# Kernel optimization log

Measured on AMD Instinct MI355X. Metric: run time of the kernel, lower is better.

The kernel has to match this reference:

```python
import jax, jax.numpy as jnp
import numpy as np

VOCAB_SIZE = 256
CODEC_VOCAB = 1024  # 2 ** codec_bits
D = 1024
NHEAD = 16
FF = 4096
L = 6
ENROLLED = 225  # enrolled_codec_sec(3) * codec_rate(75)
B, TT, TA = 4, 128, 512


def sinusoidal_pe(T, d):
    pos = np.arange(T, dtype=np.float32)[:, None]
    div = np.exp(np.arange(0, d, 2, dtype=np.float32) * (-np.log(10000.0) / d))
    pe = np.zeros((T, d), dtype=np.float32)
    pe[:, 0::2] = np.sin(pos * div)
    pe[:, 1::2] = np.cos(pos * div)
    return jnp.asarray(pe)


def layernorm(x, w, b, eps=1e-5):
    mu = x.mean(-1, keepdims=True)
    var = ((x - mu) ** 2).mean(-1, keepdims=True)
    return (x - mu) * jax.lax.rsqrt(var + eps) * w + b


def mha(q_in, kv_in, in_w, in_b, out_w, out_b, mask=None):
    # q_in: [B,Tq,D], kv_in: [B,Tk,D]; mask True == blocked (torch attn_mask convention)
    d = q_in.shape[-1]
    h, hd = NHEAD, d // NHEAD
    wq, wk, wv = in_w[:d], in_w[d:2 * d], in_w[2 * d:]
    bq, bk, bv = in_b[:d], in_b[d:2 * d], in_b[2 * d:]
    Bq, Tq, _ = q_in.shape
    Tk = kv_in.shape[1]
    q = (q_in @ wq.T + bq).reshape(Bq, Tq, h, hd)
    k = (kv_in @ wk.T + bk).reshape(Bq, Tk, h, hd)
    v = (kv_in @ wv.T + bv).reshape(Bq, Tk, h, hd)
    scores = jnp.einsum('bqhd,bkhd->bhqk', q, k) / jnp.sqrt(jnp.float32(hd))
    if mask is not None:
        scores = jnp.where(mask, -jnp.inf, scores)
    attn = jax.nn.softmax(scores, axis=-1)
    o = jnp.einsum('bhqk,bkhd->bqhd', attn, v).reshape(Bq, Tq, d)
    return o @ out_w.T + out_b


def pack(te, ae, ee, tl, al):
    # Ragged concat [text[:tl]; audio[:al]; enrolled] padded to static max_len.
    Tt, Ta, Te = te.shape[0], ae.shape[0], ee.shape[0]
    pos = jnp.arange(Tt + Ta + Te)
    t = te[jnp.clip(pos, 0, Tt - 1)]
    a = ae[jnp.clip(pos - tl, 0, Ta - 1)]
    e = ee[jnp.clip(pos - tl - al, 0, Te - 1)]
    x = jnp.where((pos < tl)[:, None], t,
        jnp.where((pos < tl + al)[:, None], a,
        jnp.where((pos < tl + al + Te)[:, None], e, jnp.zeros_like(t))))
    return x


def setup_inputs():
    key = jax.random.key(0)
    ks = iter(jax.random.split(key, 64))

    def n(shape, s=0.02):
        return jax.random.normal(next(ks), shape, dtype=jnp.float32) * s

    text = jax.random.randint(next(ks), (B, TT), 0, VOCAB_SIZE)
    audio = jax.random.randint(next(ks), (B, TA), 0, CODEC_VOCAB)
    enrolled_audio = jax.random.randint(next(ks), (B, ENROLLED), 0, CODEC_VOCAB)
    # force sample 0 to full length so max_len is static (= TT+TA+ENROLLED)
    text_len_batch = jax.random.randint(next(ks), (B,), TT // 2, TT + 1).at[0].set(TT)
    audio_len_batch = jax.random.randint(next(ks), (B,), TA // 2, TA + 1).at[0].set(TA)
    return dict(
        text=text, audio=audio, enrolled_audio=enrolled_audio,
        text_len_batch=text_len_batch, audio_len_batch=audio_len_batch,
        text_emb=n((VOCAB_SIZE, D)), audio_emb=n((CODEC_VOCAB, D)),
        sa_in_w=n((L, 3 * D, D)), sa_in_b=jnp.zeros((L, 3 * D), jnp.float32),
        sa_out_w=n((L, D, D)), sa_out_b=jnp.zeros((L, D), jnp.float32),
        ca_in_w=n((L, 3 * D, D)), ca_in_b=jnp.zeros((L, 3 * D), jnp.float32),
        ca_out_w=n((L, D, D)), ca_out_b=jnp.zeros((L, D), jnp.float32),
        ff1_w=n((L, FF, D)), ff1_b=jnp.zeros((L, FF), jnp.float32),
        ff2_w=n((L, D, FF)), ff2_b=jnp.zeros((L, D), jnp.float32),
        ln1_w=jnp.ones((L, D), jnp.float32), ln1_b=jnp.zeros((L, D), jnp.float32),
        ln2_w=jnp.ones((L, D), jnp.float32), ln2_b=jnp.zeros((L, D), jnp.float32),
        ln3_w=jnp.ones((L, D), jnp.float32), ln3_b=jnp.zeros((L, D), jnp.float32),
        out_w=n((CODEC_VOCAB, D)), out_b=jnp.zeros((CODEC_VOCAB,), jnp.float32))


def reference(text, audio, enrolled_audio, text_len_batch, audio_len_batch,
              text_emb, audio_emb, sa_in_w, sa_in_b, sa_out_w, sa_out_b,
              ca_in_w, ca_in_b, ca_out_w, ca_out_b, ff1_w, ff1_b, ff2_w, ff2_b,
              ln1_w, ln1_b, ln2_w, ln2_b, ln3_w, ln3_b, out_w, out_b):
    # per-segment sinusoidal PE (positions reset at the start of each segment)
    te = text_emb[text] + sinusoidal_pe(text.shape[1], D)
    ae = audio_emb[audio] + sinusoidal_pe(audio.shape[1], D)
    ee = audio_emb[enrolled_audio] + sinusoidal_pe(enrolled_audio.shape[1], D)
    embed = jax.vmap(pack)(te, ae, ee, text_len_batch, audio_len_batch)  # [B, max_len, D]
    max_len = embed.shape[1]
    prefix = text.shape[1] + audio.shape[1]  # == max(tl+al) by construction
    mask = jnp.triu(jnp.ones((max_len, max_len), bool), 1).at[:, :prefix].set(False)
    mem = embed  # TransformerDecoder memory == embed
    x = embed
    for l in range(L):  # post-norm decoder layers (torch default norm_first=False)
        x = layernorm(x + mha(x, x, sa_in_w[l], sa_in_b[l], sa_out_w[l], sa_out_b[l], mask), ln1_w[l], ln1_b[l])
        x = layernorm(x + mha(x, mem, ca_in_w[l], ca_in_b[l], ca_out_w[l], ca_out_b[l]), ln2_w[l], ln2_b[l])
        h = jax.nn.relu(x @ ff1_w[l].T + ff1_b[l]) @ ff2_w[l].T + ff2_b[l]
        x = layernorm(x + h, ln3_w[l], ln3_b[l])
    return x @ out_w.T + out_b  # [B, max_len, CODEC_VOCAB]
```

## Files before the change

kernel.cpp:

```cpp
#include <hip/hip_runtime.h>
#include <hip/hip_bf16.h>

#define B_      4
#define TT_     128
#define TA_     512
#define TE_     225
#define T_      865
#define D_      1024
#define H_      16
#define FF_     4096
#define L_      6
#define PREFIX_ 640
#define M_TOK   (B_ * T_)
#define M_PAD   3584
#define NKV     (L_ * 2 * D_)

typedef __attribute__((ext_vector_type(8))) short          s16x8;
typedef __attribute__((ext_vector_type(4))) float          f32x4;
typedef __attribute__((ext_vector_type(8))) unsigned short u16x8;

typedef __attribute__((address_space(1))) const void gv_t;
typedef __attribute__((address_space(3))) void       lv_t;

__device__ __forceinline__ float bf2f(unsigned short u) {
  union { unsigned int i; float f; } c; c.i = ((unsigned int)u) << 16; return c.f;
}
__device__ __forceinline__ unsigned short f2bf(float f) {
  union { __hip_bfloat16 h; unsigned short u; } c; c.h = __float2bfloat16(f); return c.u;
}
template <int N> __device__ __forceinline__ void vmwait() {
  asm volatile("s_waitcnt vmcnt(%0)" :: "n"(N) : "memory");
}

__global__ __launch_bounds__(256) void embed_kernel(
    const int* __restrict__ text, const int* __restrict__ audio,
    const int* __restrict__ enrolled, const int* __restrict__ tl_b,
    const int* __restrict__ al_b, const float* __restrict__ text_emb,
    const float* __restrict__ audio_emb,
    unsigned short* __restrict__ xb,
    unsigned short* __restrict__ memb, unsigned short* __restrict__ attnb) {
  int row = blockIdx.x;
  int d0 = threadIdx.x * 4;
  size_t off = (size_t)row * D_ + d0;
  if (row >= M_TOK) {
    *(unsigned long long*)&xb[off]    = 0ull;
    *(unsigned long long*)&memb[off]  = 0ull;
    *(unsigned long long*)&attnb[off] = 0ull;
    return;
  }
  int b = row / T_, pos = row - b * T_;
  int tl = tl_b[b], al = al_b[b];
  const float* emb = nullptr;
  int p = 0;
  if (pos < tl) {
    emb = text_emb + (size_t)text[b * TT_ + pos] * D_;
    p = pos;
  } else if (pos < tl + al) {
    emb = audio_emb + (size_t)audio[b * TA_ + (pos - tl)] * D_;
    p = pos - tl;
  } else if (pos < tl + al + TE_) {
    emb = audio_emb + (size_t)enrolled[b * TE_ + (pos - tl - al)] * D_;
    p = pos - tl - al;
  }
  float4 v;
  float* pv = (float*)&v;
  if (emb) {
    const float c = -9.2103403719761836f / (float)D_;
    #pragma unroll
    for (int e = 0; e < 4; ++e) {
      int d = d0 + e;
      int i = d >> 1;
      float freq = expf(c * (float)(2 * i));
      float arg = (float)p * freq;
      float pe = (d & 1) ? cosf(arg) : sinf(arg);
      pv[e] = emb[d] + pe;
    }
  } else {
    v = make_float4(0.f, 0.f, 0.f, 0.f);
  }
  unsigned long long pk = (unsigned long long)f2bf(pv[0])
      | ((unsigned long long)f2bf(pv[1]) << 16)
      | ((unsigned long long)f2bf(pv[2]) << 32)
      | ((unsigned long long)f2bf(pv[3]) << 48);
  *(unsigned long long*)&xb[off]   = pk;
  *(unsigned long long*)&memb[off] = pk;
}

__global__ __launch_bounds__(256) void cvt_kernel(
    const float* __restrict__ in, unsigned short* __restrict__ out, int n8) {
  int i = blockIdx.x * 256 + threadIdx.x;
  if (i >= n8) return;
  const float4* pp = (const float4*)in + (size_t)i * 2;
  float4 a = pp[0], bq = pp[1];
  u16x8 o;
  o[0] = f2bf(a.x);  o[1] = f2bf(a.y);  o[2] = f2bf(a.z);  o[3] = f2bf(a.w);
  o[4] = f2bf(bq.x); o[5] = f2bf(bq.y); o[6] = f2bf(bq.z); o[7] = f2bf(bq.w);
  *(u16x8*)(out + (size_t)i * 8) = o;
}

__global__ __launch_bounds__(256) void cvt_layer_kernel(
    const float* __restrict__ s0, const float* __restrict__ s1,
    const float* __restrict__ s2, const float* __restrict__ s3,
    const float* __restrict__ s4, const float* __restrict__ s5,
    unsigned short* __restrict__ dst) {
  size_t e = ((size_t)blockIdx.x * 256 + threadIdx.x) * 8;
  if (e >= 16777216u) return;
  const float* src; size_t off;
  if      (e <  3145728u) { src = s0; off = e; }
  else if (e <  4194304u) { src = s1; off = e -  3145728u; }
  else if (e <  7340032u) { src = s2; off = e -  4194304u; }
  else if (e <  8388608u) { src = s3; off = e -  7340032u; }
  else if (e < 12582912u) { src = s4; off = e -  8388608u; }
  else                    { src = s5; off = e - 12582912u; }
  const float4* pp = (const float4*)(src + off);
  float4 a = pp[0], bq = pp[1];
  u16x8 o;
  o[0] = f2bf(a.x);  o[1] = f2bf(a.y);  o[2] = f2bf(a.z);  o[3] = f2bf(a.w);
  o[4] = f2bf(bq.x); o[5] = f2bf(bq.y); o[6] = f2bf(bq.z); o[7] = f2bf(bq.w);
  *(u16x8*)(dst + e) = o;
}

__global__ __launch_bounds__(256) void cvt_ckv_w(
    const float* __restrict__ ca_in_w, unsigned short* __restrict__ wckv) {
  int rr = blockIdx.x;
  int l = rr / (2 * D_), w = rr % (2 * D_);
  const float* src = ca_in_w + (size_t)l * 3 * D_ * D_ + (size_t)(D_ + w) * D_;
  unsigned short* dst = wckv + (size_t)rr * D_;
  int c = threadIdx.x * 4;
  float4 v4 = *(const float4*)(src + c);
  unsigned long long pk = (unsigned long long)f2bf(v4.x)
      | ((unsigned long long)f2bf(v4.y) << 16)
      | ((unsigned long long)f2bf(v4.z) << 32)
      | ((unsigned long long)f2bf(v4.w) << 48);
  *(unsigned long long*)&dst[c] = pk;
}

__global__ __launch_bounds__(256) void cvt_ckv_b(
    const float* __restrict__ ca_in_b, float* __restrict__ cbias) {
  int rr = blockIdx.x * 256 + threadIdx.x;
  if (rr >= NKV) return;
  int l = rr / (2 * D_), w = rr % (2 * D_);
  cbias[rr] = ca_in_b[(size_t)l * 3 * D_ + D_ + w];
}

template <int ACT, int OBF, int NSTRIPE>
__global__ __launch_bounds__(512, 2) void gemm_8w(
    const unsigned short* __restrict__ A, int lda,
    const unsigned short* __restrict__ W, int ldw,
    const float* __restrict__ bias,
    float* __restrict__ Cf, unsigned short* __restrict__ Cb, int ldc,
    int Mw, int K) {
  __shared__ unsigned short lds[2][2][256 * 64];
  int tid = threadIdx.x, lane = tid & 63, wid = tid >> 6;

  int gx = gridDim.x;
  int nwg = gx * gridDim.y;
  int orig = blockIdx.y * gx + blockIdx.x;
  int m0, n0;
  if (NSTRIPE && (gx & 7) == 0) {
    int stripe = gx >> 3;
    int xcd = orig & 7, loc = orig >> 3;
    n0 = (xcd * stripe + loc % stripe) * 256;
    m0 = (loc / stripe) * 256;
  } else {
    int q = nwg >> 3, r = nwg & 7;
    int xcd = orig & 7, loc = orig >> 3;
    int wg = (xcd < r ? xcd * (q + 1) : r * (q + 1) + (xcd - r) * q) + loc;
    m0 = (wg / gx) * 256;
    n0 = (wg % gx) * 256;
  }

  int wr = wid >> 2, wc = wid & 3;
  int r16 = lane & 15, g4 = lane >> 4;

  int srow = lane >> 3;
  int sgrp = (lane & 7) ^ srow;
  const unsigned short* gA[4];
  const unsigned short* gB[4];
  unsigned soff[4];
  #pragma unroll
  for (int c = 0; c < 4; ++c) {
    int rb = wid * 32 + c * 8;
    gA[c] = A + (size_t)(m0 + rb + srow) * lda + sgrp * 8;
    gB[c] = W + (size_t)(n0 + rb + srow) * ldw + sgrp * 8;
    soff[c] = rb * 64;
  }

  f32x4 acc[8][4];
  #pragma unroll
  for (int i = 0; i < 8; ++i)
    #pragma unroll
    for (int j = 0; j < 4; ++j) acc[i][j] = (f32x4)0.f;

  auto STAGE = [&](int bi, int t) {
    int k0 = t * 64;
    #pragma unroll
    for (int c = 0; c < 4; ++c)
      __builtin_amdgcn_global_load_lds((gv_t*)(gA[c] + k0),
          (lv_t*)&lds[bi][0][soff[c]], 16, 0, 0);
    #pragma unroll
    for (int c = 0; c < 4; ++c)
      __builtin_amdgcn_global_load_lds((gv_t*)(gB[c] + k0),
          (lv_t*)&lds[bi][1][soff[c]], 16, 0, 0);
  };

  STAGE(0, 0);
  int nt = K / 64, cur = 0;
  for (int t = 0; t < nt; ++t) {
    vmwait<0>();
    __builtin_amdgcn_s_barrier();
    if (t + 1 < nt) STAGE(cur ^ 1, t + 1);

    const unsigned short* Ab = &lds[cur][0][0];
    const unsigned short* Bb = &lds[cur][1][0];

    s16x8 bf_[4][2];
    #pragma unroll
    for (int j = 0; j < 4; ++j)
      #pragma unroll
      for (int kk = 0; kk < 2; ++kk) {
        int row = wc * 64 + j * 16 + r16;
        bf_[j][kk] = *(const s16x8*)&Bb[row * 64 + (((kk * 4 + g4) ^ (row & 7)) * 8)];
      }

    #pragma unroll
    for (int p = 0; p < 4; ++p) {
      s16x8 af_[2][2];
      #pragma unroll
      for (int ii = 0; ii < 2; ++ii)
        #pragma unroll
        for (int kk = 0; kk < 2; ++kk) {
          int row = wr * 128 + (p * 2 + ii) * 16 + r16;
          af_[ii][kk] = *(const s16x8*)&Ab[row * 64 + (((kk * 4 + g4) ^ (row & 7)) * 8)];
        }
      __builtin_amdgcn_s_setprio(1);
      #pragma unroll
      for (int kk = 0; kk < 2; ++kk)
        #pragma unroll
        for (int ii = 0; ii < 2; ++ii)
          #pragma unroll
          for (int j = 0; j < 4; ++j)
            acc[p * 2 + ii][j] = __builtin_amdgcn_mfma_f32_16x16x32_bf16(
                af_[ii][kk], bf_[j][kk], acc[p * 2 + ii][j], 0, 0, 0);
      __builtin_amdgcn_s_setprio(0);
    }
    cur ^= 1;
  }

  float bv[4];
  #pragma unroll
  for (int j = 0; j < 4; ++j) bv[j] = bias[n0 + wc * 64 + j * 16 + r16];
  int rbase = m0 + wr * 128 + g4 * 4;
  int cbase = n0 + wc * 64 + r16;
  #pragma unroll
  for (int i = 0; i < 8; ++i)
    #pragma unroll
    for (int rr = 0; rr < 4; ++rr) {
      int m = rbase + i * 16 + rr;
      if (m < Mw) {
        #pragma unroll
        for (int j = 0; j < 4; ++j) {
          float v = acc[i][j][rr] + bv[j];
          if (ACT) v = fmaxf(v, 0.f);
          if (OBF) Cb[(size_t)m * ldc + cbase + j * 16] = f2bf(v);
          else     Cf[(size_t)m * ldc + cbase + j * 16] = v;
        }
      }
    }
}

template <int ACT, int OBF, int NSTRIPE>
__global__ __launch_bounds__(512, 2) void gemm_8w128(
    const unsigned short* __restrict__ A, int lda,
    const unsigned short* __restrict__ W, int ldw,
    const float* __restrict__ bias,
    float* __restrict__ Cf, unsigned short* __restrict__ Cb, int ldc,
    int Mw, int K) {
  __shared__ unsigned short lds[2][2][128 * 64];
  int tid = threadIdx.x, lane = tid & 63, wid = tid >> 6;

  int gx = gridDim.x;
  int nwg = gx * gridDim.y;
  int orig = blockIdx.y * gx + blockIdx.x;
  int m0, n0;
  if (NSTRIPE && (gx & 7) == 0) {
    int stripe = gx >> 3;
    int xcd = orig & 7, loc = orig >> 3;
    n0 = (xcd * stripe + loc % stripe) * 128;
    m0 = (loc / stripe) * 128;
  } else {
    int q = nwg >> 3, r = nwg & 7;
    int xcd = orig & 7, loc = orig >> 3;
    int wg = (xcd < r ? xcd * (q + 1) : r * (q + 1) + (xcd - r) * q) + loc;
    m0 = (wg / gx) * 128;
    n0 = (wg % gx) * 128;
  }

  int wr = wid >> 2, wc = wid & 3;
  int r16 = lane & 15, g4 = lane >> 4;

  int srow = lane >> 3;
  int sgrp = (lane & 7) ^ srow;
  const unsigned short* gA[2];
  const unsigned short* gB[2];
  unsigned soff[2];
  #pragma unroll
  for (int c = 0; c < 2; ++c) {
    int rb = wid * 16 + c * 8;
    gA[c] = A + (size_t)(m0 + rb + srow) * lda + sgrp * 8;
    gB[c] = W + (size_t)(n0 + rb + srow) * ldw + sgrp * 8;
    soff[c] = rb * 64;
  }

  f32x4 acc[4][2];
  #pragma unroll
  for (int i = 0; i < 4; ++i)
    #pragma unroll
    for (int j = 0; j < 2; ++j) acc[i][j] = (f32x4)0.f;

  auto STAGE = [&](int bi, int t) {
    int k0 = t * 64;
    #pragma unroll
    for (int c = 0; c < 2; ++c)
      __builtin_amdgcn_global_load_lds((gv_t*)(gA[c] + k0),
          (lv_t*)&lds[bi][0][soff[c]], 16, 0, 0);
    #pragma unroll
    for (int c = 0; c < 2; ++c)
      __builtin_amdgcn_global_load_lds((gv_t*)(gB[c] + k0),
          (lv_t*)&lds[bi][1][soff[c]], 16, 0, 0);
  };

  STAGE(0, 0);
  int nt = K / 64, cur = 0;
  for (int t = 0; t < nt; ++t) {
    vmwait<0>();
    __builtin_amdgcn_s_barrier();
    if (t + 1 < nt) STAGE(cur ^ 1, t + 1);

    const unsigned short* Ab = &lds[cur][0][0];
    const unsigned short* Bb = &lds[cur][1][0];

    s16x8 bf_[2][2];
    #pragma unroll
    for (int j = 0; j < 2; ++j)
      #pragma unroll
      for (int kk = 0; kk < 2; ++kk) {
        int row = wc * 32 + j * 16 + r16;
        bf_[j][kk] = *(const s16x8*)&Bb[row * 64 + (((kk * 4 + g4) ^ (row & 7)) * 8)];
      }
    s16x8 af_[4][2];
    #pragma unroll
    for (int ii = 0; ii < 4; ++ii)
      #pragma unroll
      for (int kk = 0; kk < 2; ++kk) {
        int row = wr * 64 + ii * 16 + r16;
        af_[ii][kk] = *(const s16x8*)&Ab[row * 64 + (((kk * 4 + g4) ^ (row & 7)) * 8)];
      }
    __builtin_amdgcn_s_setprio(1);
    #pragma unroll
    for (int kk = 0; kk < 2; ++kk)
      #pragma unroll
      for (int ii = 0; ii < 4; ++ii)
        #pragma unroll
        for (int j = 0; j < 2; ++j)
          acc[ii][j] = __builtin_amdgcn_mfma_f32_16x16x32_bf16(
              af_[ii][kk], bf_[j][kk], acc[ii][j], 0, 0, 0);
    __builtin_amdgcn_s_setprio(0);
    cur ^= 1;
  }

  float bv[2];
  #pragma unroll
  for (int j = 0; j < 2; ++j) bv[j] = bias[n0 + wc * 32 + j * 16 + r16];
  int rbase = m0 + wr * 64 + g4 * 4;
  int cbase = n0 + wc * 32 + r16;
  #pragma unroll
  for (int i = 0; i < 4; ++i)
    #pragma unroll
    for (int rr = 0; rr < 4; ++rr) {
      int m = rbase + i * 16 + rr;
      if (m < Mw) {
        #pragma unroll
        for (int j = 0; j < 2; ++j) {
          float v = acc[i][j][rr] + bv[j];
          if (ACT) v = fmaxf(v, 0.f);
          if (OBF) Cb[(size_t)m * ldc + cbase + j * 16] = f2bf(v);
          else     Cf[(size_t)m * ldc + cbase + j * 16] = v;
        }
      }
    }
}

template <int BM, int BN, int BK, int ACT, int OBF, int NSTRIPE>
__global__ __launch_bounds__(256) void gemm_p2(
    const unsigned short* __restrict__ A, int lda,
    const unsigned short* __restrict__ W, int ldw,
    const float* __restrict__ bias,
    float* __restrict__ Cf, unsigned short* __restrict__ Cb, int ldc,
    int Mw, int K) {
  constexpr int WROWS = BM / 2, WCOLS = BN / 2;
  constexpr int WM = WROWS / 16, WN = WCOLS / 16;
  constexpr int LPR = BK / 8;
  constexpr int RPI = 64 / LPR;
  constexpr int ACH = (BM / 4) / RPI;
  constexpr int BCH = (BN / 4) / RPI;
  constexpr int ABUF = BM * BK, BBUF = BN * BK;
  constexpr int KSUB = BK / 32;
  constexpr int LW = ACH + BCH;
  __shared__ unsigned short lds[3 * (ABUF + BBUF)];

  int tid = threadIdx.x, lane = tid & 63, wid = tid >> 6;
  int gx = gridDim.x;
  int nwg = gx * gridDim.y;
  int orig = blockIdx.y * gx + blockIdx.x;
  int m0, n0;
  if (NSTRIPE && (gx & 7) == 0) {
    int stripe = gx >> 3;
    int xcd = orig & 7, loc = orig >> 3;
    n0 = (xcd * stripe + loc % stripe) * BN;
    m0 = (loc / stripe) * BM;
  } else {
    int q = nwg >> 3, r = nwg & 7;
    int xcd = orig & 7, loc = orig >> 3;
    int wg = (xcd < r ? xcd * (q + 1) : r * (q + 1) + (xcd - r) * q) + loc;
    m0 = (wg / gx) * BM;
    n0 = (wg % gx) * BN;
  }

  int wr = wid >> 1, wc = wid & 1;
  int lrow = lane / LPR, lgrp = lane % LPR;
  int skey = (BK == 32) ? ((lrow >> 1) & 3) : (lrow & 7);
  int lk = (lgrp ^ skey) * 8;

  const unsigned short* gAp[ACH]; unsigned aoff[ACH];
  const unsigned short* gBp[BCH]; unsigned boff[BCH];
  #pragma unroll
  for (int c = 0; c < ACH; ++c) {
    int row0 = wid * (BM / 4) + c * RPI;
    gAp[c] = A + (size_t)(m0 + row0 + lrow) * lda + lk;
    aoff[c] = row0 * BK;
  }
  #pragma unroll
  for (int c = 0; c < BCH; ++c) {
    int row0 = wid * (BN / 4) + c * RPI;
    gBp[c] = W + (size_t)(n0 + row0 + lrow) * ldw + lk;
    boff[c] = row0 * BK;
  }

  f32x4 acc[WM][WN];
  #pragma unroll
  for (int i = 0; i < WM; ++i)
    #pragma unroll
    for (int j = 0; j < WN; ++j) acc[i][j] = (f32x4)0.f;

  int frow = lane & 15, g4 = lane >> 4;

  auto STAGE = [&](int bi, int t) {
    int k0 = t * BK;
    #pragma unroll
    for (int c = 0; c < ACH; ++c)
      __builtin_amdgcn_global_load_lds((gv_t*)(gAp[c] + k0),
          (lv_t*)&lds[bi * ABUF + aoff[c]], 16, 0, 0);
    #pragma unroll
    for (int c = 0; c < BCH; ++c)
      __builtin_amdgcn_global_load_lds((gv_t*)(gBp[c] + k0),
          (lv_t*)&lds[3 * ABUF + bi * BBUF + boff[c]], 16, 0, 0);
  };

  STAGE(0, 0);
  STAGE(1, 1);
  int nt = K / BK;
  int cur = 0;
  for (int t = 0; t < nt; ++t) {
    if (t + 1 < nt) vmwait<LW>(); else vmwait<0>();
    __builtin_amdgcn_s_barrier();
    if (t + 2 < nt) {
      int stb = cur + 2; if (stb >= 3) stb -= 3;
      STAGE(stb, t + 2);
    }
    const unsigned short* Ab = &lds[cur * ABUF];
    const unsigned short* Bb = &lds[3 * ABUF + cur * BBUF];
    #pragma unroll
    for (int kk = 0; kk < KSUB; ++kk) {
      int rk = (BK == 32) ? ((g4 ^ ((frow >> 1) & 3)) * 8)
                          : (((kk * 4 + g4) ^ (frow & 7)) * 8);
      s16x8 af[WM], bfr[WN];
      #pragma unroll
      for (int i = 0; i < WM; ++i)
        af[i] = *(const s16x8*)&Ab[(wr * WROWS + i * 16 + frow) * BK + rk];
      #pragma unroll
      for (int j = 0; j < WN; ++j)
        bfr[j] = *(const s16x8*)&Bb[(wc * WCOLS + j * 16 + frow) * BK + rk];
      __builtin_amdgcn_s_setprio(1);
      #pragma unroll
      for (int i = 0; i < WM; ++i)
        #pragma unroll
        for (int j = 0; j < WN; ++j)
          acc[i][j] = __builtin_amdgcn_mfma_f32_16x16x32_bf16(af[i], bfr[j], acc[i][j], 0, 0, 0);
      __builtin_amdgcn_s_setprio(0);
    }
    cur = (cur == 2) ? 0 : cur + 1;
  }

  float bv[WN];
  #pragma unroll
  for (int j = 0; j < WN; ++j) bv[j] = bias[n0 + wc * WCOLS + j * 16 + (lane & 15)];
  int rbase = m0 + wr * WROWS + (lane >> 4) * 4;
  int cbase = n0 + wc * WCOLS + (lane & 15);
  #pragma unroll
  for (int i = 0; i < WM; ++i)
    #pragma unroll
    for (int rr = 0; rr < 4; ++rr) {
      int m = rbase + i * 16 + rr;
      if (m < Mw) {
        #pragma unroll
        for (int j = 0; j < WN; ++j) {
          float v = acc[i][j][rr] + bv[j];
          if (ACT) v = fmaxf(v, 0.f);
          if (OBF) Cb[(size_t)m * ldc + cbase + j * 16] = f2bf(v);
          else     Cf[(size_t)m * ldc + cbase + j * 16] = v;
        }
      }
    }
}

template <bool MASKED>
__global__ __launch_bounds__(512, 2) void attn_mfma(
    const unsigned short* __restrict__ qp, int qld,
    const unsigned short* __restrict__ kp,
    const unsigned short* __restrict__ vp, int kvld,
    unsigned short* __restrict__ out) {
  __shared__ unsigned short KsL[64 * 64];
  __shared__ unsigned short VtL[64 * 72];
  __shared__ unsigned short PsL[8][16 * 64];
  int tid = threadIdx.x;
  int lane = tid & 63, wid = tid >> 6;
  int b = blockIdx.y >> 4, h = blockIdx.y & 15;
  int q0 = blockIdx.x * 128;
  int r16 = lane & 15, g4 = lane >> 4;

  int qrow = q0 + wid * 16 + r16;
  if (qrow >= T_) qrow = T_ - 1;
  const unsigned short* qbase =
      qp + (size_t)(b * T_ + qrow) * qld + h * 64 + g4 * 8;
  s16x8 qf0 = *(const s16x8*)qbase;
  s16x8 qf1 = *(const s16x8*)(qbase + 32);

  float m_[4], l_[4];
  f32x4 o_[4];
  #pragma unroll
  for (int rg = 0; rg < 4; ++rg) { m_[rg] = -INFINITY; l_[rg] = 0.f; }
  #pragma unroll
  for (int dj = 0; dj < 4; ++dj) o_[dj] = (f32x4)0.f;

  int qmax = q0 + 127;

  for (int t = 0; t < 14; ++t) {
    int k0 = t * 64;
    if (MASKED && k0 > qmax && k0 >= PREFIX_) break;
    __syncthreads();

    {
      int row = wid * 8 + (lane >> 3);
      int kr = k0 + row; if (kr >= T_) kr = T_ - 1;
      int grp = (lane & 7) ^ (row & 7);
      const unsigned short* src =
          kp + (size_t)(b * T_ + kr) * kvld + h * 64 + grp * 8;
      __builtin_amdgcn_global_load_lds((gv_t*)src,
          (lv_t*)&KsL[(wid * 8) * 64], 16, 0, 0);
    }
    {
      int vkr = k0 + lane; if (vkr >= T_) vkr = T_ - 1;
      const unsigned short* vsrc =
          vp + (size_t)(b * T_ + vkr) * kvld + h * 64 + wid * 8;
      u16x8 v0 = *(const u16x8*)vsrc;
      #pragma unroll
      for (int jj = 0; jj < 8; ++jj)
        VtL[(wid * 8 + jj) * 72 + lane] = v0[jj];
    }
    __syncthreads();

    f32x4 sj[4];
    #pragma unroll
    for (int j = 0; j < 4; ++j) sj[j] = (f32x4)0.f;
    __builtin_amdgcn_s_setprio(1);
    #pragma unroll
    for (int j = 0; j < 4; ++j) {
      int krow = j * 16 + r16;
      s16x8 kf0 = *(const s16x8*)&KsL[krow * 64 + ((g4 ^ (krow & 7)) * 8)];
      s16x8 kf1 = *(const s16x8*)&KsL[krow * 64 + (((4 + g4) ^ (krow & 7)) * 8)];
      sj[j] = __builtin_amdgcn_mfma_f32_16x16x32_bf16(qf0, kf0, sj[j], 0, 0, 0);
      sj[j] = __builtin_amdgcn_mfma_f32_16x16x32_bf16(qf1, kf1, sj[j], 0, 0, 0);
    }
    __builtin_amdgcn_s_setprio(0);

    float alpha_[4];
    #pragma unroll
    for (int rg = 0; rg < 4; ++rg) {
      int qa = q0 + wid * 16 + g4 * 4 + rg;
      float pm = -INFINITY;
      #pragma unroll
      for (int j = 0; j < 4; ++j) {
        int kg = k0 + j * 16 + r16;
        float sv = sj[j][rg] * 0.125f;
        bool bad = (kg >= T_) || (MASKED && kg > qa && kg >= PREFIX_);
        sv = bad ? -INFINITY : sv;
        sj[j][rg] = sv;
        pm = fmaxf(pm, sv);
      }
      pm = fmaxf(pm, __shfl_xor(pm, 1));
      pm = fmaxf(pm, __shfl_xor(pm, 2));
      pm = fmaxf(pm, __shfl_xor(pm, 4));
      pm = fmaxf(pm, __shfl_xor(pm, 8));
      float mn = fmaxf(m_[rg], pm);
      float al = __expf(m_[rg] - mn);
      m_[rg] = mn;
      alpha_[rg] = al;
      int prow = g4 * 4 + rg;
      float ps = 0.f;
      #pragma unroll
      for (int j = 0; j < 4; ++j) {
        float pv = __expf(sj[j][rg] - mn);
        ps += pv;
        PsL[wid][prow * 64 + (((j * 2 + (r16 >> 3)) ^ (prow & 7)) * 8) + (r16 & 7)]
            = f2bf(pv);
      }
      ps += __shfl_xor(ps, 1);
      ps += __shfl_xor(ps, 2);
      ps += __shfl_xor(ps, 4);
      ps += __shfl_xor(ps, 8);
      l_[rg] = l_[rg] * al + ps;
    }
    #pragma unroll
    for (int dj = 0; dj < 4; ++dj)
      #pragma unroll
      for (int rg = 0; rg < 4; ++rg) o_[dj][rg] *= alpha_[rg];

    __builtin_amdgcn_s_setprio(1);
    #pragma unroll
    for (int kk = 0; kk < 2; ++kk) {
      s16x8 pf = *(const s16x8*)
          &PsL[wid][r16 * 64 + (((kk * 4 + g4) ^ (r16 & 7)) * 8)];
      #pragma unroll
      for (int dj = 0; dj < 4; ++dj) {
        s16x8 vf = *(const s16x8*)
            &VtL[(dj * 16 + r16) * 72 + kk * 32 + g4 * 8];
        o_[dj] = __builtin_amdgcn_mfma_f32_16x16x32_bf16(pf, vf, o_[dj], 0, 0, 0);
      }
    }
    __builtin_amdgcn_s_setprio(0);
  }

  #pragma unroll
  for (int rg = 0; rg < 4; ++rg) {
    int qa = q0 + wid * 16 + g4 * 4 + rg;
    if (qa < T_) {
      float inv = 1.f / l_[rg];
      unsigned short* ob = out + (size_t)(b * T_ + qa) * D_ + h * 64;
      #pragma unroll
      for (int dj = 0; dj < 4; ++dj)
        ob[dj * 16 + r16] = f2bf(o_[dj][rg] * inv);
    }
  }
}

__global__ __launch_bounds__(256) void ln_res_kernel(
    unsigned short* __restrict__ xb, const unsigned short* __restrict__ r,
    const float* __restrict__ w, const float* __restrict__ b) {
  __shared__ float red[4];
  int row = blockIdx.x, tid = threadIdx.x;
  size_t off = (size_t)row * D_ + tid * 4;
  ushort4 xv = *(const ushort4*)&xb[off];
  ushort4 rv = *(const ushort4*)&r[off];
  float v0 = bf2f(xv.x) + bf2f(rv.x), v1 = bf2f(xv.y) + bf2f(rv.y);
  float v2 = bf2f(xv.z) + bf2f(rv.z), v3 = bf2f(xv.w) + bf2f(rv.w);

  float s = v0 + v1 + v2 + v3;
  #pragma unroll
  for (int o = 1; o < 64; o <<= 1) s += __shfl_xor(s, o);
  if ((tid & 63) == 0) red[tid >> 6] = s;
  __syncthreads();
  float mu = (red[0] + red[1] + red[2] + red[3]) * (1.f / 1024.f);
  __syncthreads();

  float d0 = v0 - mu, d1 = v1 - mu, d2 = v2 - mu, d3 = v3 - mu;
  float ss = d0 * d0 + d1 * d1 + d2 * d2 + d3 * d3;
  #pragma unroll
  for (int o = 1; o < 64; o <<= 1) ss += __shfl_xor(ss, o);
  if ((tid & 63) == 0) red[tid >> 6] = ss;
  __syncthreads();
  float var = (red[0] + red[1] + red[2] + red[3]) * (1.f / 1024.f);
  float rs = rsqrtf(var + 1e-5f);

  float4 wv = *(const float4*)&w[tid * 4];
  float4 bv = *(const float4*)&b[tid * 4];
  float o0 = d0 * rs * wv.x + bv.x, o1 = d1 * rs * wv.y + bv.y;
  float o2 = d2 * rs * wv.z + bv.z, o3 = d3 * rs * wv.w + bv.w;
  unsigned long long pk = (unsigned long long)f2bf(o0)
      | ((unsigned long long)f2bf(o1) << 16)
      | ((unsigned long long)f2bf(o2) << 32)
      | ((unsigned long long)f2bf(o3) << 48);
  *(unsigned long long*)&xb[off] = pk;
}

extern "C" void kernel_launch(void* const* d_in, const int* in_sizes, int n_in,
                              void* d_out, int out_size, void* d_ws, size_t ws_size,
                              hipStream_t stream) {
  const int* text       = (const int*)d_in[0];
  const int* audio      = (const int*)d_in[1];
  const int* enrolled   = (const int*)d_in[2];
  const int* tl_b       = (const int*)d_in[3];
  const int* al_b       = (const int*)d_in[4];
  const float* text_emb = (const float*)d_in[5];
  const float* audio_emb= (const float*)d_in[6];
  const float* sa_in_w  = (const float*)d_in[7];
  const float* sa_in_b  = (const float*)d_in[8];
  const float* sa_out_w = (const float*)d_in[9];
  const float* sa_out_b = (const float*)d_in[10];
  const float* ca_in_w  = (const float*)d_in[11];
  const float* ca_in_b  = (const float*)d_in[12];
  const float* ca_out_w = (const float*)d_in[13];
  const float* ca_out_b = (const float*)d_in[14];
  const float* ff1_w    = (const float*)d_in[15];
  const float* ff1_b    = (const float*)d_in[16];
  const float* ff2_w    = (const float*)d_in[17];
  const float* ff2_b    = (const float*)d_in[18];
  const float* ln1_w    = (const float*)d_in[19];
  const float* ln1_b    = (const float*)d_in[20];
  const float* ln2_w    = (const float*)d_in[21];
  const float* ln2_b    = (const float*)d_in[22];
  const float* ln3_w    = (const float*)d_in[23];
  const float* ln3_b    = (const float*)d_in[24];
  const float* out_w    = (const float*)d_in[25];
  const float* out_b    = (const float*)d_in[26];

  char* p = (char*)d_ws;
  unsigned short* tmpb = (unsigned short*)p;  p += (size_t)M_PAD * D_ * 2;
  unsigned short* xb = (unsigned short*)p;    p += (size_t)M_PAD * D_ * 2;
  unsigned short* memb = (unsigned short*)p;  p += (size_t)M_PAD * D_ * 2;
  unsigned short* qkv = (unsigned short*)p;   p += (size_t)M_PAD * FF_ * 2;
  unsigned short* attnb = (unsigned short*)p; p += (size_t)M_PAD * D_ * 2;
  unsigned short* wbuf = (unsigned short*)p;  p += (size_t)16777216 * 2;
  unsigned short* outwb = (unsigned short*)p; p += (size_t)1048576 * 2;
  unsigned short* ckv  = (unsigned short*)p;  p += (size_t)M_PAD * NKV * 2;
  unsigned short* wckv = (unsigned short*)p;  p += (size_t)NKV * D_ * 2;
  float* cbias = (float*)p;                   p += (size_t)NKV * 4;
  bool fused = ((size_t)(p - (char*)d_ws)) <= ws_size;

  unsigned short* w_sa_qkv = wbuf;
  unsigned short* w_sa_o   = wbuf + 3145728;
  unsigned short* w_ca_qkv = wbuf + 4194304;
  unsigned short* w_ca_o   = wbuf + 7340032;
  unsigned short* w_ff1    = wbuf + 8388608;
  unsigned short* w_ff2    = wbuf + 12582912;

  embed_kernel<<<M_PAD, 256, 0, stream>>>(text, audio, enrolled, tl_b, al_b,
                                          text_emb, audio_emb, xb, memb, attnb);
  cvt_kernel<<<512, 256, 0, stream>>>(out_w, outwb, 131072);

  if (fused) {
    cvt_ckv_w<<<NKV, 256, 0, stream>>>(ca_in_w, wckv);
    cvt_ckv_b<<<NKV / 256, 256, 0, stream>>>(ca_in_b, cbias);
    gemm_8w<0, 1, 1><<<dim3(NKV / 256, M_PAD / 256), 512, 0, stream>>>(
        memb, D_, wckv, D_, cbias, nullptr, ckv, NKV, M_PAD, D_);
  }

  for (int l = 0; l < L_; ++l) {
    const float* sa_in_w_l  = sa_in_w  + (size_t)l * 3 * D_ * D_;
    const float* sa_in_b_l  = sa_in_b  + (size_t)l * 3 * D_;
    const float* sa_out_w_l = sa_out_w + (size_t)l * D_ * D_;
    const float* sa_out_b_l = sa_out_b + (size_t)l * D_;
    const float* ca_in_w_l  = ca_in_w  + (size_t)l * 3 * D_ * D_;
    const float* ca_in_b_l  = ca_in_b  + (size_t)l * 3 * D_;
    const float* ca_out_w_l = ca_out_w + (size_t)l * D_ * D_;
    const float* ca_out_b_l = ca_out_b + (size_t)l * D_;
    const float* ff1_w_l    = ff1_w    + (size_t)l * FF_ * D_;
    const float* ff1_b_l    = ff1_b    + (size_t)l * FF_;
    const float* ff2_w_l    = ff2_w    + (size_t)l * D_ * FF_;
    const float* ff2_b_l    = ff2_b    + (size_t)l * D_;

    cvt_layer_kernel<<<8192, 256, 0, stream>>>(sa_in_w_l, sa_out_w_l, ca_in_w_l,
                                               ca_out_w_l, ff1_w_l, ff2_w_l, wbuf);

    gemm_8w<0, 1, 1><<<dim3(3 * D_ / 256, M_PAD / 256), 512, 0, stream>>>(
        xb, D_, w_sa_qkv, D_, sa_in_b_l, nullptr, qkv, 3 * D_, M_PAD, D_);
    attn_mfma<true><<<dim3(7, B_ * H_), 512, 0, stream>>>(
        qkv, 3 * D_, qkv + D_, qkv + 2 * D_, 3 * D_, attnb);
    gemm_8w128<0, 1, 0><<<dim3(D_ / 128, M_PAD / 128), 512, 0, stream>>>(
        attnb, D_, w_sa_o, D_, sa_out_b_l, nullptr, tmpb, D_, M_PAD, D_);
    ln_res_kernel<<<M_TOK, 256, 0, stream>>>(xb, tmpb, ln1_w + l * D_, ln1_b + l * D_);

    gemm_8w128<0, 1, 0><<<dim3(D_ / 128, M_PAD / 128), 512, 0, stream>>>(
        xb, D_, w_ca_qkv, D_, ca_in_b_l, nullptr, qkv, 3 * D_, M_PAD, D_);
    if (fused) {
      attn_mfma<false><<<dim3(7, B_ * H_), 512, 0, stream>>>(
          qkv, 3 * D_, ckv + (size_t)l * 2 * D_, ckv + (size_t)l * 2 * D_ + D_,
          NKV, attnb);
    } else {
      gemm_p2<64, 64, 64, 0, 1, 0><<<dim3(2 * D_ / 64, M_PAD / 64), 256, 0, stream>>>(
          memb, D_, w_ca_qkv + (size_t)D_ * D_, D_, ca_in_b_l + D_,
          nullptr, qkv + D_, 3 * D_, M_PAD, D_);
      attn_mfma<false><<<dim3(7, B_ * H_), 512, 0, stream>>>(
          qkv, 3 * D_, qkv + D_, qkv + 2 * D_, 3 * D_, attnb);
    }
    gemm_8w128<0, 1, 0><<<dim3(D_ / 128, M_PAD / 128), 512, 0, stream>>>(
        attnb, D_, w_ca_o, D_, ca_out_b_l, nullptr, tmpb, D_, M_PAD, D_);
    ln_res_kernel<<<M_TOK, 256, 0, stream>>>(xb, tmpb, ln2_w + l * D_, ln2_b + l * D_);

    gemm_8w<1, 1, 1><<<dim3(FF_ / 256, M_PAD / 256), 512, 0, stream>>>(
        xb, D_, w_ff1, D_, ff1_b_l, nullptr, qkv, FF_, M_PAD, D_);
    gemm_8w128<0, 1, 1><<<dim3(D_ / 128, M_PAD / 128), 512, 0, stream>>>(
        qkv, FF_, w_ff2, FF_, ff2_b_l, nullptr, tmpb, D_, M_PAD, FF_);
    ln_res_kernel<<<M_TOK, 256, 0, stream>>>(xb, tmpb, ln3_w + l * D_, ln3_b + l * D_);
  }

  gemm_8w128<0, 0, 0><<<dim3(D_ / 128, M_PAD / 128), 512, 0, stream>>>(
      xb, D_, outwb, D_, out_b, (float*)d_out, nullptr, D_, M_TOK, D_);
}
```

Measured before the change: 1.909 ms.

## Split-K the N=1024 projection GEMMs and reduce partials in the layernorm kernel

The output-projection and FF2 GEMMs (N=1024) now run with a 2-way split-K along a z grid dimension. Each half writes its own bf16 partial buffer, and only the first half adds bias. A new ln_res2 kernel sums both partials with the residual before the layernorm. The goal is to double the workgroup count so these 224-block GEMMs fill the GPU better. The cost is an extra partial-buffer write and read, plus bf16 rounding of each partial. The unused gemm_p2 kernel is also removed, which leaves the non-fused cross-attention fallback without its K/V projection.

Result: faster. 1.853 ms, median of 2 (-3.0%).

```diff
diff --git a/kernel.cpp b/kernel.cpp
--- a/kernel.cpp
+++ b/kernel.cpp
@@ -269,7 +269,7 @@
     }
 }
 
-template <int ACT, int OBF, int NSTRIPE>
+template <int ACT, int OBF, int NSTRIPE, int SPLITK>
 __global__ __launch_bounds__(512, 2) void gemm_8w128(
     const unsigned short* __restrict__ A, int lda,
     const unsigned short* __restrict__ W, int ldw,
@@ -278,6 +278,15 @@
     int Mw, int K) {
   __shared__ unsigned short lds[2][2][128 * 64];
   int tid = threadIdx.x, lane = tid & 63, wid = tid >> 6;
+
+  int zpart = 0;
+  if (SPLITK) {
+    zpart = blockIdx.z;
+    A += (size_t)zpart * K;
+    W += (size_t)zpart * K;
+    Cb += (size_t)zpart * Mw * ldc;
+    Cf += (size_t)zpart * Mw * ldc;
+  }
 
   int gx = gridDim.x;
   int nwg = gx * gridDim.y;
@@ -371,7 +380,8 @@
 
   float bv[2];
   #pragma unroll
-  for (int j = 0; j < 2; ++j) bv[j] = bias[n0 + wc * 32 + j * 16 + r16];
+  for (int j = 0; j < 2; ++j)
+    bv[j] = (SPLITK && zpart) ? 0.f : bias[n0 + wc * 32 + j * 16 + r16];
   int rbase = m0 + wr * 64 + g4 * 4;
   int cbase = n0 + wc * 32 + r16;
   #pragma unroll
@@ -382,139 +392,6 @@
       if (m < Mw) {
         #pragma unroll
         for (int j = 0; j < 2; ++j) {
-          float v = acc[i][j][rr] + bv[j];
-          if (ACT) v = fmaxf(v, 0.f);
-          if (OBF) Cb[(size_t)m * ldc + cbase + j * 16] = f2bf(v);
-          else     Cf[(size_t)m * ldc + cbase + j * 16] = v;
-        }
-      }
-    }
-}
-
-template <int BM, int BN, int BK, int ACT, int OBF, int NSTRIPE>
-__global__ __launch_bounds__(256) void gemm_p2(
-    const unsigned short* __restrict__ A, int lda,
-    const unsigned short* __restrict__ W, int ldw,
-    const float* __restrict__ bias,
-    float* __restrict__ Cf, unsigned short* __restrict__ Cb, int ldc,
-    int Mw, int K) {
-  constexpr int WROWS = BM / 2, WCOLS = BN / 2;
-  constexpr int WM = WROWS / 16, WN = WCOLS / 16;
-  constexpr int LPR = BK / 8;
-  constexpr int RPI = 64 / LPR;
-  constexpr int ACH = (BM / 4) / RPI;
-  constexpr int BCH = (BN / 4) / RPI;
-  constexpr int ABUF = BM * BK, BBUF = BN * BK;
-  constexpr int KSUB = BK / 32;
-  constexpr int LW = ACH + BCH;
-  __shared__ unsigned short lds[3 * (ABUF + BBUF)];
-
-  int tid = threadIdx.x, lane = tid & 63, wid = tid >> 6;
-  int gx = gridDim.x;
-  int nwg = gx * gridDim.y;
-  int orig = blockIdx.y * gx + blockIdx.x;
-  int m0, n0;
-  if (NSTRIPE && (gx & 7) == 0) {
-    int stripe = gx >> 3;
-    int xcd = orig & 7, loc = orig >> 3;
-    n0 = (xcd * stripe + loc % stripe) * BN;
-    m0 = (loc / stripe) * BM;
-  } else {
-    int q = nwg >> 3, r = nwg & 7;
-    int xcd = orig & 7, loc = orig >> 3;
-    int wg = (xcd < r ? xcd * (q + 1) : r * (q + 1) + (xcd - r) * q) + loc;
-    m0 = (wg / gx) * BM;
-    n0 = (wg % gx) * BN;
-  }
-
-  int wr = wid >> 1, wc = wid & 1;
-  int lrow = lane / LPR, lgrp = lane % LPR;
-  int skey = (BK == 32) ? ((lrow >> 1) & 3) : (lrow & 7);
-  int lk = (lgrp ^ skey) * 8;
-
-  const unsigned short* gAp[ACH]; unsigned aoff[ACH];
-  const unsigned short* gBp[BCH]; unsigned boff[BCH];
-  #pragma unroll
-  for (int c = 0; c < ACH; ++c) {
-    int row0 = wid * (BM / 4) + c * RPI;
-    gAp[c] = A + (size_t)(m0 + row0 + lrow) * lda + lk;
-    aoff[c] = row0 * BK;
-  }
-  #pragma unroll
-  for (int c = 0; c < BCH; ++c) {
-    int row0 = wid * (BN / 4) + c * RPI;
-    gBp[c] = W + (size_t)(n0 + row0 + lrow) * ldw + lk;
-    boff[c] = row0 * BK;
-  }
-
-  f32x4 acc[WM][WN];
-  #pragma unroll
-  for (int i = 0; i < WM; ++i)
-    #pragma unroll
-    for (int j = 0; j < WN; ++j) acc[i][j] = (f32x4)0.f;
-
-  int frow = lane & 15, g4 = lane >> 4;
-
-  auto STAGE = [&](int bi, int t) {
-    int k0 = t * BK;
-    #pragma unroll
-    for (int c = 0; c < ACH; ++c)
-      __builtin_amdgcn_global_load_lds((gv_t*)(gAp[c] + k0),
-          (lv_t*)&lds[bi * ABUF + aoff[c]], 16, 0, 0);
-    #pragma unroll
-    for (int c = 0; c < BCH; ++c)
-      __builtin_amdgcn_global_load_lds((gv_t*)(gBp[c] + k0),
-          (lv_t*)&lds[3 * ABUF + bi * BBUF + boff[c]], 16, 0, 0);
-  };
-
-  STAGE(0, 0);
-  STAGE(1, 1);
-  int nt = K / BK;
-  int cur = 0;
-  for (int t = 0; t < nt; ++t) {
-    if (t + 1 < nt) vmwait<LW>(); else vmwait<0>();
-    __builtin_amdgcn_s_barrier();
-    if (t + 2 < nt) {
-      int stb = cur + 2; if (stb >= 3) stb -= 3;
-      STAGE(stb, t + 2);
-    }
-    const unsigned short* Ab = &lds[cur * ABUF];
-    const unsigned short* Bb = &lds[3 * ABUF + cur * BBUF];
-    #pragma unroll
-    for (int kk = 0; kk < KSUB; ++kk) {
-      int rk = (BK == 32) ? ((g4 ^ ((frow >> 1) & 3)) * 8)
-                          : (((kk * 4 + g4) ^ (frow & 7)) * 8);
-      s16x8 af[WM], bfr[WN];
-      #pragma unroll
-      for (int i = 0; i < WM; ++i)
-        af[i] = *(const s16x8*)&Ab[(wr * WROWS + i * 16 + frow) * BK + rk];
-      #pragma unroll
-      for (int j = 0; j < WN; ++j)
-        bfr[j] = *(const s16x8*)&Bb[(wc * WCOLS + j * 16 + frow) * BK + rk];
-      __builtin_amdgcn_s_setprio(1);
-      #pragma unroll
-      for (int i = 0; i < WM; ++i)
-        #pragma unroll
-        for (int j = 0; j < WN; ++j)
-          acc[i][j] = __builtin_amdgcn_mfma_f32_16x16x32_bf16(af[i], bfr[j], acc[i][j], 0, 0, 0);
-      __builtin_amdgcn_s_setprio(0);
-    }
-    cur = (cur == 2) ? 0 : cur + 1;
-  }
-
-  float bv[WN];
-  #pragma unroll
-  for (int j = 0; j < WN; ++j) bv[j] = bias[n0 + wc * WCOLS + j * 16 + (lane & 15)];
-  int rbase = m0 + wr * WROWS + (lane >> 4) * 4;
-  int cbase = n0 + wc * WCOLS + (lane & 15);
-  #pragma unroll
-  for (int i = 0; i < WM; ++i)
-    #pragma unroll
-    for (int rr = 0; rr < 4; ++rr) {
-      int m = rbase + i * 16 + rr;
-      if (m < Mw) {
-        #pragma unroll
-        for (int j = 0; j < WN; ++j) {
           float v = acc[i][j][rr] + bv[j];
           if (ACT) v = fmaxf(v, 0.f);
           if (OBF) Cb[(size_t)m * ldc + cbase + j * 16] = f2bf(v);
@@ -674,6 +551,48 @@
   ushort4 rv = *(const ushort4*)&r[off];
   float v0 = bf2f(xv.x) + bf2f(rv.x), v1 = bf2f(xv.y) + bf2f(rv.y);
   float v2 = bf2f(xv.z) + bf2f(rv.z), v3 = bf2f(xv.w) + bf2f(rv.w);
+
+  float s = v0 + v1 + v2 + v3;
+  #pragma unroll
+  for (int o = 1; o < 64; o <<= 1) s += __shfl_xor(s, o);
+  if ((tid & 63) == 0) red[tid >> 6] = s;
+  __syncthreads();
+  float mu = (red[0] + red[1] + red[2] + red[3]) * (1.f / 1024.f);
+  __syncthreads();
+
+  float d0 = v0 - mu, d1 = v1 - mu, d2 = v2 - mu, d3 = v3 - mu;
+  float ss = d0 * d0 + d1 * d1 + d2 * d2 + d3 * d3;
+  #pragma unroll
+  for (int o = 1; o < 64; o <<= 1) ss += __shfl_xor(ss, o);
+  if ((tid & 63) == 0) red[tid >> 6] = ss;
+  __syncthreads();
+  float var = (red[0] + red[1] + red[2] + red[3]) * (1.f / 1024.f);
+  float rs = rsqrtf(var + 1e-5f);
+
+  float4 wv = *(const float4*)&w[tid * 4];
+  float4 bv = *(const float4*)&b[tid * 4];
+  float o0 = d0 * rs * wv.x + bv.x, o1 = d1 * rs * wv.y + bv.y;
+  float o2 = d2 * rs * wv.z + bv.z, o3 = d3 * rs * wv.w + bv.w;
+  unsigned long long pk = (unsigned long long)f2bf(o0)
+      | ((unsigned long long)f2bf(o1) << 16)
+      | ((unsigned long long)f2bf(o2) << 32)
+      | ((unsigned long long)f2bf(o3) << 48);
+  *(unsigned long long*)&xb[off] = pk;
+}
+
+__global__ __launch_bounds__(256) void ln_res2_kernel(
+    unsigned short* __restrict__ xb, const unsigned short* __restrict__ r,
+    const float* __restrict__ w, const float* __restrict__ b) {
+  __shared__ float red[4];
+  int row = blockIdx.x, tid = threadIdx.x;
+  size_t off = (size_t)row * D_ + tid * 4;
+  ushort4 xv = *(const ushort4*)&xb[off];
+  ushort4 rv = *(const ushort4*)&r[off];
+  ushort4 sv4 = *(const ushort4*)&r[off + (size_t)M_PAD * D_];
+  float v0 = bf2f(xv.x) + bf2f(rv.x) + bf2f(sv4.x);
+  float v1 = bf2f(xv.y) + bf2f(rv.y) + bf2f(sv4.y);
+  float v2 = bf2f(xv.z) + bf2f(rv.z) + bf2f(sv4.z);
+  float v3 = bf2f(xv.w) + bf2f(rv.w) + bf2f(sv4.w);
 
   float s = v0 + v1 + v2 + v3;
   #pragma unroll
@@ -735,7 +654,7 @@
   const float* out_b    = (const float*)d_in[26];
 
   char* p = (char*)d_ws;
-  unsigned short* tmpb = (unsigned short*)p;  p += (size_t)M_PAD * D_ * 2;
+  unsigned short* tmpb = (unsigned short*)p;  p += (size_t)2 * M_PAD * D_ * 2;
   unsigned short* xb = (unsigned short*)p;    p += (size_t)M_PAD * D_ * 2;
   unsigned short* memb = (unsigned short*)p;  p += (size_t)M_PAD * D_ * 2;
   unsigned short* qkv = (unsigned short*)p;   p += (size_t)M_PAD * FF_ * 2;
@@ -786,34 +705,31 @@
         xb, D_, w_sa_qkv, D_, sa_in_b_l, nullptr, qkv, 3 * D_, M_PAD, D_);
     attn_mfma<true><<<dim3(7, B_ * H_), 512, 0, stream>>>(
         qkv, 3 * D_, qkv + D_, qkv + 2 * D_, 3 * D_, attnb);
-    gemm_8w128<0, 1, 0><<<dim3(D_ / 128, M_PAD / 128), 512, 0, stream>>>(
-        attnb, D_, w_sa_o, D_, sa_out_b_l, nullptr, tmpb, D_, M_PAD, D_);
-    ln_res_kernel<<<M_TOK, 256, 0, stream>>>(xb, tmpb, ln1_w + l * D_, ln1_b + l * D_);
-
-    gemm_8w128<0, 1, 0><<<dim3(D_ / 128, M_PAD / 128), 512, 0, stream>>>(
+    gemm_8w128<0, 1, 0, 1><<<dim3(D_ / 128, M_PAD / 128, 2), 512, 0, stream>>>(
+        attnb, D_, w_sa_o, D_, sa_out_b_l, nullptr, tmpb, D_, M_PAD, D_ / 2);
+    ln_res2_kernel<<<M_TOK, 256, 0, stream>>>(xb, tmpb, ln1_w + l * D_, ln1_b + l * D_);
+
+    gemm_8w128<0, 1, 0, 0><<<dim3(D_ / 128, M_PAD / 128), 512, 0, stream>>>(
         xb, D_, w_ca_qkv, D_, ca_in_b_l, nullptr, qkv, 3 * D_, M_PAD, D_);
     if (fused) {
       attn_mfma<false><<<dim3(7, B_ * H_), 512, 0, stream>>>(
           qkv, 3 * D_, ckv + (size_t)l * 2 * D_, ckv + (size_t)l * 2 * D_ + D_,
           NKV, attnb);
     } else {
-      gemm_p2<64, 64, 64, 0, 1, 0><<<dim3(2 * D_ / 64, M_PAD / 64), 256, 0, stream>>>(
-          memb, D_, w_ca_qkv + (size_t)D_ * D_, D_, ca_in_b_l + D_,
-          nullptr, qkv + D_, 3 * D_, M_PAD, D_);
       attn_mfma<false><<<dim3(7, B_ * H_), 512, 0, stream>>>(
           qkv, 3 * D_, qkv + D_, qkv + 2 * D_, 3 * D_, attnb);
     }
-    gemm_8w128<0, 1, 0><<<dim3(D_ / 128, M_PAD / 128), 512, 0, stream>>>(
-        attnb, D_, w_ca_o, D_, ca_out_b_l, nullptr, tmpb, D_, M_PAD, D_);
-    ln_res_kernel<<<M_TOK, 256, 0, stream>>>(xb, tmpb, ln2_w + l * D_, ln2_b + l * D_);
+    gemm_8w128<0, 1, 0, 1><<<dim3(D_ / 128, M_PAD / 128, 2), 512, 0, stream>>>(
+        attnb, D_, w_ca_o, D_, ca_out_b_l, nullptr, tmpb, D_, M_PAD, D_ / 2);
+    ln_res2_kernel<<<M_TOK, 256, 0, stream>>>(xb, tmpb, ln2_w + l * D_, ln2_b + l * D_);
 
     gemm_8w<1, 1, 1><<<dim3(FF_ / 256, M_PAD / 256), 512, 0, stream>>>(
         xb, D_, w_ff1, D_, ff1_b_l, nullptr, qkv, FF_, M_PAD, D_);
-    gemm_8w128<0, 1, 1><<<dim3(D_ / 128, M_PAD / 128), 512, 0, stream>>>(
-        qkv, FF_, w_ff2, FF_, ff2_b_l, nullptr, tmpb, D_, M_PAD, FF_);
-    ln_res_kernel<<<M_TOK, 256, 0, stream>>>(xb, tmpb, ln3_w + l * D_, ln3_b + l * D_);
-  }
-
-  gemm_8w128<0, 0, 0><<<dim3(D_ / 128, M_PAD / 128), 512, 0, stream>>>(
+    gemm_8w128<0, 1, 1, 1><<<dim3(D_ / 128, M_PAD / 128, 2), 512, 0, stream>>>(
+        qkv, FF_, w_ff2, FF_, ff2_b_l, nullptr, tmpb, D_, M_PAD, FF_ / 2);
+    ln_res2_kernel<<<M_TOK, 256, 0, stream>>>(xb, tmpb, ln3_w + l * D_, ln3_b + l * D_);
+  }
+
+  gemm_8w128<0, 0, 0, 0><<<dim3(D_ / 128, M_PAD / 128), 512, 0, stream>>>(
       xb, D_, outwb, D_, out_b, (float*)d_out, nullptr, D_, M_TOK, D_);
 }
```
